# Performance work log

Hardware: AMD Instinct MI355X
Metric: run time of the kernel (lower is better)

The kernel has to match this reference:

```python
import jax, jax.numpy as jnp
import numpy as np

NS, NV = 48, 10                    # scalar / vector multiplicities (cfg.ns, cfg.nv)
WN = NS * NS + NS * NV             # per-edge TP weight numel: paths 0e*0e->0e and 0e*1o->1o
OUT = NS + 3 * NV                  # out irreps 48x0e + 10x1o -> 78 dims
INV = float(1.0 / np.sqrt(NS))     # e3nn-style path normalization (fan_in = mul_in)
N_LIG, N_REC, N_ATOM = 2000, 2000, 15000
E_LL, E_RR, E_AA = 15000, 10000, 15000
E_LR, E_LA, E_AR = 5000, 8000, 8000


def setup_inputs() -> dict:
    key = jax.random.key(0)
    ks = jax.random.split(key, 40)
    f = lambda i, shape, s=1.0: jax.random.normal(ks[i], shape, dtype=jnp.float32) * s
    ii = lambda i, n, e: jax.random.randint(ks[i], (e,), 0, n, dtype=jnp.int32)
    w_s = (1.0 / (3 * NS)) ** 0.5
    return {
        'lig_x': f(0, (N_LIG, NS)), 'rec_x': f(1, (N_REC, NS)), 'atom_x': f(2, (N_ATOM, NS)),
        'll_attr': f(3, (E_LL, NS)), 'rr_attr': f(4, (E_RR, NS)), 'aa_attr': f(5, (E_AA, NS)),
        'lr_attr': f(6, (E_LR, NS)), 'la_attr': f(7, (E_LA, NS)), 'ar_attr': f(8, (E_AR, NS)),
        'll_sh': f(9, (E_LL, 9)), 'rr_sh': f(10, (E_RR, 9)), 'aa_sh': f(11, (E_AA, 9)),
        'lr_sh': f(12, (E_LR, 9)), 'la_sh': f(13, (E_LA, 9)), 'ar_sh': f(14, (E_AR, 9)),
        'mlp_w1': f(15, (9, 3 * NS, 3 * NS), w_s), 'mlp_b1': jnp.zeros((9, 3 * NS), jnp.float32),
        'mlp_w2': f(16, (9, 3 * NS, 3 * NS), w_s), 'mlp_b2': jnp.zeros((9, 3 * NS), jnp.float32),
        'mlp_w3': f(17, (9, 3 * NS, WN), w_s), 'mlp_b3': jnp.zeros((9, WN), jnp.float32),
        'll_src': ii(18, N_LIG, E_LL), 'll_dst': ii(19, N_LIG, E_LL),
        'rr_src': ii(20, N_REC, E_RR), 'rr_dst': ii(21, N_REC, E_RR),
        'aa_src': ii(22, N_ATOM, E_AA), 'aa_dst': ii(23, N_ATOM, E_AA),
        'lr_lig': ii(24, N_LIG, E_LR), 'lr_rec': ii(25, N_REC, E_LR),
        'la_lig': ii(26, N_LIG, E_LA), 'la_atom': ii(27, N_ATOM, E_LA),
        'ar_atom': ii(28, N_ATOM, E_AR), 'ar_rec': ii(29, N_REC, E_AR),
    }


def _tp_conv(src_x, dst_x, e_attr, e_sh, src_idx, dst_idx, n_dst, w1, b1, w2, b2, w3, b3):
    """FullyConnectedTensorProductConv: per-edge MLP -> TP weights, CG tensor
    product of gathered source features with edge SH, mean scatter to dst."""
    fs = src_x[src_idx]                                          # (E, ns) gather
    z = jnp.concatenate([e_attr, fs, dst_x[dst_idx]], axis=-1)
    h = jax.nn.relu(z @ w1 + b1)
    h = jax.nn.relu(h @ w2 + b2)
    w = h @ w3 + b3                                              # (E, WN) edge-conditioned TP weights
    w0 = w[:, : NS * NS].reshape(-1, NS, NS)                     # 0e x 0e -> 0e path
    wv = w[:, NS * NS :].reshape(-1, NS, NV)                     # 0e x 1o -> 1o path
    out0 = jnp.einsum('ei,eio->eo', fs, w0) * e_sh[:, :1] * INV  # (E, ns)
    outv = jnp.einsum('ei,eiv,em->evm', fs, wv, e_sh[:, 1:4]) * INV  # (E, nv, 3)
    msg = jnp.concatenate([out0, outv.reshape(-1, NV * 3)], axis=-1)
    agg = jax.ops.segment_sum(msg, dst_idx, num_segments=n_dst)
    deg = jax.ops.segment_sum(jnp.ones((msg.shape[0], 1), msg.dtype), dst_idx, num_segments=n_dst)
    return agg / jnp.maximum(deg, 1.0)                           # mean reduction


def reference(lig_x, rec_x, atom_x, ll_attr, rr_attr, aa_attr, lr_attr, la_attr, ar_attr,
              ll_sh, rr_sh, aa_sh, lr_sh, la_sh, ar_sh,
              mlp_w1, mlp_b1, mlp_w2, mlp_b2, mlp_w3, mlp_b3,
              ll_src, ll_dst, rr_src, rr_dst, aa_src, aa_dst,
              lr_lig, lr_rec, la_lig, la_atom, ar_atom, ar_rec):
    P = lambda c: (mlp_w1[c], mlp_b1[c], mlp_w2[c], mlp_b2[c], mlp_w3[c], mlp_b3[c])
    # one interaction layer = 9 structurally distinct convs (lig/rec/atom intra + 6 cross dirs)
    lig_u = (_tp_conv(lig_x, lig_x, ll_attr, ll_sh, ll_src, ll_dst, N_LIG, *P(0))
           + _tp_conv(rec_x, lig_x, lr_attr, lr_sh, lr_rec, lr_lig, N_LIG, *P(1))
           + _tp_conv(atom_x, lig_x, la_attr, la_sh, la_atom, la_lig, N_LIG, *P(2)))
    rec_u = (_tp_conv(lig_x, rec_x, lr_attr, lr_sh, lr_lig, lr_rec, N_REC, *P(3))
           + _tp_conv(rec_x, rec_x, rr_attr, rr_sh, rr_src, rr_dst, N_REC, *P(4))
           + _tp_conv(atom_x, rec_x, ar_attr, ar_sh, ar_atom, ar_rec, N_REC, *P(5)))
    atom_u = (_tp_conv(lig_x, atom_x, la_attr, la_sh, la_lig, la_atom, N_ATOM, *P(6))
            + _tp_conv(rec_x, atom_x, ar_attr, ar_sh, ar_rec, ar_atom, N_ATOM, *P(7))
            + _tp_conv(atom_x, atom_x, aa_attr, aa_sh, aa_src, aa_dst, N_ATOM, *P(8)))
    pad = lambda x: jnp.pad(x, ((0, 0), (0, OUT - NS)))          # residual: pad scalars to out irreps
    return jnp.concatenate([pad(lig_x) + lig_u, pad(rec_x) + rec_u, pad(atom_x) + atom_u], axis=0)
```

## Files before the change

kernel.cpp:

```cpp
#include <hip/hip_runtime.h>


namespace {

constexpr int NCONV = 9;
constexpr int ETOT  = 82000;
constexpr float INV = 0.14433756729740643f;

constexpr int EC[NCONV]     = {15000,5000,8000,5000,10000,8000,8000,8000,15000};
constexpr int NBLKC[NCONV]  = {118,40,63,40,79,63,63,63,118};
constexpr int EOFF[NCONV]   = {0,15000,20000,28000,33000,43000,51000,59000,67000};
constexpr int DEGOFF[NCONV] = {0,2000,4000,6000,8000,10000,12000,27000,42000};
constexpr int NODEC[NCONV]  = {2000,2000,2000,2000,2000,2000,15000,15000,15000};
constexpr int NBLK_TOT = 647;

typedef _Float16 f16;
typedef __attribute__((ext_vector_type(8))) _Float16 f16x8;
typedef __attribute__((ext_vector_type(4))) _Float16 f16x4;
typedef __attribute__((ext_vector_type(4))) float f32x4;

#define MFMA(a, b, c) __builtin_amdgcn_mfma_f32_16x16x32_f16((a), (b), (c), 0, 0, 0)

struct ConvPtrs {
  const float* src_x[NCONV];
  const float* dst_x[NCONV];
  const float* attr[NCONV];
  const float* sh[NCONV];
  const int*   sidx[NCONV];
  const int*   didx[NCONV];
};

}

__device__ __forceinline__ int xcd_remap(int bid) {
  const int xcd = bid & 7, slot = bid >> 3;
  return (xcd <= 6) ? (xcd * 81 + slot) : (567 + slot);
}

__device__ __forceinline__ int conv_decode(int bid, int& rem) {
  int c = 0; rem = bid;
  while (c < NCONV - 1 && rem >= NBLKC[c]) { rem -= NBLKC[c]; ++c; }
  return c;
}

__device__ __forceinline__ void gld_lds16(const void* g, void* l) {
  __builtin_amdgcn_global_load_lds(
      (const __attribute__((address_space(1))) void*)g,
      (__attribute__((address_space(3))) void*)l, 16, 0, 0);
}

__device__ __forceinline__ f32x4 cvt4(f16x4 h) {
  return (f32x4){(float)h[0], (float)h[1], (float)h[2], (float)h[3]};
}

__global__ __launch_bounds__(256) void prep_all(
    ConvPtrs P,
    const float* __restrict__ w1, const float* __restrict__ b1,
    const float* __restrict__ w2, const float* __restrict__ b2,
    const float* __restrict__ w3, const float* __restrict__ b3,
    f16* __restrict__ w1f, f16* __restrict__ w2f, f16* __restrict__ w3f,
    float* __restrict__ deg) {
  __shared__ float W[145][60];
  const int blk = blockIdx.x;
  if (blk < 203) {
    const int unit = blk * 4 + (threadIdx.x >> 6);
    if (unit >= 810) return;
    const int l = threadIdx.x & 63;
    const int sel = unit >= 405, bb = sel ? unit - 405 : unit;
    const int c = bb / 45, r2 = bb % 45, cb = r2 / 5, s = r2 % 5;
    const float* w  = sel ? w2 : w1;
    const float* bi = sel ? b2 : b1;
    f16* dst = (sel ? w2f : w1f) + ((size_t)(c * 9 + cb) * 5 + s) * 512;
    const int n = cb * 16 + (l & 15);
    f16x8 pack;
#pragma unroll
    for (int j = 0; j < 8; ++j) {
      const int k = s * 32 + ((l >> 4) << 3) + j;
      float v = 0.f;
      if (k < 144)       v = w[((size_t)c * 144 + k) * 144 + n];
      else if (k == 144) v = bi[c * 144 + n];
      pack[j] = (f16)v;
    }
    ((f16x8*)dst)[l] = pack;
  } else if (blk < 635) {
    const int b = blk - 203;
    const int c = b / 48, i = b % 48;
    const float* wc = w3 + (size_t)c * 144 * 2784;
    const float* bc = b3 + (size_t)c * 2784;
    for (int u = threadIdx.x; u < 145 * 58; u += 256) {
      const int row = u / 58, t = u - row * 58;
      const int col = (t < 48) ? (i * 48 + t) : (2304 + i * 10 + (t - 48));
      const float* src = (row == 144) ? bc : (wc + (size_t)row * 2784);
      W[row][t] = src[col];
    }
    __syncthreads();
    f16* dst = w3f + (size_t)(c * 48 + i) * 20 * 512;
#pragma unroll 1
    for (int it = 0; it < 40; ++it) {
      const int f = it * 256 + threadIdx.x;
      const int s = f >> 11, g2 = f & 2047, cb = g2 >> 9, l = (g2 >> 3) & 63, j = f & 7;
      const int k = s * 32 + ((l >> 4) << 3) + j;
      const int col = cb * 16 + (l & 15);
      const float v = (k <= 144 && col < 58) ? W[k][col] : 0.f;
      dst[f] = (f16)v;
    }
  } else {
    const int gid = (blk - 635) * 256 + threadIdx.x;
    if (gid >= ETOT) return;
    int c = 0;
    while (c < NCONV - 1 && gid >= EOFF[c + 1]) ++c;
    const int e = gid - EOFF[c];
    atomicAdd(&deg[DEGOFF[c] + P.didx[c][e]], 1.0f);
  }
}

__global__ __launch_bounds__(256) void scan_kernel(
    const float* __restrict__ deg, int* __restrict__ offs, int* __restrict__ cursor) {
  __shared__ int part[256];
  const int c = blockIdx.x, N = NODEC[c], base = DEGOFF[c];
  const int tid = threadIdx.x;
  const int chunk = (N + 255) / 256;
  const int start = tid * chunk;
  const int end = (start + chunk < N) ? (start + chunk) : N;
  int s = 0;
  for (int i = start; i < end; ++i) s += (int)deg[base + i];
  part[tid] = s;
  __syncthreads();
  if (tid == 0) {
    int acc = 0;
    for (int k = 0; k < 256; ++k) { int t = part[k]; part[k] = acc; acc += t; }
  }
  __syncthreads();
  int acc = part[tid];
  for (int i = start; i < end; ++i) {
    offs[base + i] = acc; cursor[base + i] = acc;
    acc += (int)deg[base + i];
  }
}

__global__ __launch_bounds__(256) void slot_kernel(
    ConvPtrs P, int* __restrict__ cursor, int* __restrict__ inv_slot) {
  const int gid = blockIdx.x * 256 + threadIdx.x;
  if (gid >= ETOT) return;
  int c = 0;
  while (c < NCONV - 1 && gid >= EOFF[c + 1]) ++c;
  const int e = gid - EOFF[c];
  const int d = P.didx[c][e];
  inv_slot[gid] = atomicAdd(&cursor[DEGOFF[c] + d], 1);
}

template<int NCB, int CB0>
__device__ __forceinline__ void layer_mm(
    const f16x8* __restrict__ Av, const f16x8* __restrict__ wv,
    int c, int lane, int wr, f32x4 acc[4][5]) {
#pragma unroll
  for (int rb = 0; rb < 4; ++rb)
#pragma unroll
    for (int cb = 0; cb < NCB; ++cb) acc[rb][cb] = (f32x4)0.0f;
#pragma unroll
  for (int s = 0; s < 5; ++s) {
    f16x8 B[NCB];
#pragma unroll
    for (int cb = 0; cb < NCB; ++cb)
      B[cb] = wv[((size_t)(c * 9 + CB0 + cb) * 5 + s) * 64 + lane];
    f16x8 A[4];
#pragma unroll
    for (int rb = 0; rb < 4; ++rb) A[rb] = Av[((wr * 4 + rb) * 5 + s) * 64 + lane];
#pragma unroll
    for (int rb = 0; rb < 4; ++rb)
#pragma unroll
      for (int cb = 0; cb < NCB; ++cb)
        acc[rb][cb] = MFMA(A[rb], B[cb], acc[rb][cb]);
  }
}

template<int NCB, int CB0>
__device__ __forceinline__ void layer_wb(const f32x4 acc[4][5], f16* __restrict__ At,
                                         int lane, int wr) {
#pragma unroll
  for (int cb = 0; cb < NCB; ++cb) {
    const int k = (CB0 + cb) * 16 + (lane & 15);
    const int s = k >> 5, g = (k >> 3) & 3, j = k & 7;
#pragma unroll
    for (int rb = 0; rb < 4; ++rb)
#pragma unroll
      for (int r = 0; r < 4; ++r) {
        const int row = ((lane >> 4) << 2) + r;
        At[((((wr * 4 + rb) * 5 + s) * 4 + g) * 16 + row) * 8 + j] =
            (f16)fmaxf(acc[rb][cb][r], 0.f);
      }
  }
}

__global__ __launch_bounds__(256, 3) void fused_conv(
    ConvPtrs P, const f16* __restrict__ w1f, const f16* __restrict__ w2f,
    const f16* __restrict__ w3f, const float* __restrict__ deg,
    const int* __restrict__ inv_slot, f16* __restrict__ medge) {
  __shared__ __align__(16) char smem[54272];
  f16* Atile = (f16*)smem;
  f16 (*fst)[128] = (f16 (*)[128])(smem + 40960);
  int* sidb = (int*)(smem + 53248);
  int* dstb = (int*)(smem + 53760);

  int rem; const int c = conv_decode(xcd_remap(blockIdx.x), rem);
  const int E = EC[c], e0 = rem * 128;
  const int tid = threadIdx.x, lane = tid & 63, w = tid >> 6;
  const int wr = w >> 1, wc = w & 1;

  if (tid < 128) {
    int ec = e0 + tid; if (ec >= E) ec = E - 1;
    sidb[tid] = P.sidx[c][ec];
    dstb[tid] = P.didx[c][ec];
  }
  __syncthreads();

  {
    const float* attr = P.attr[c];
    const float* sx = P.src_x[c];
    const float* dx = P.dst_x[c];
#pragma unroll 1
    for (int it = 0; it < 10; ++it) {
      const int u = it * 256 + tid, j8 = u >> 7, e = u & 127;
      int ec = e0 + e; if (ec >= E) ec = E - 1;
      float v[8];
      if (j8 < 6) {
        const float* p = attr + (size_t)ec * 48 + j8 * 8;
#pragma unroll
        for (int t = 0; t < 8; ++t) v[t] = p[t];
      } else if (j8 < 12) {
        const float* p = sx + (size_t)sidb[e] * 48 + (j8 - 6) * 8;
#pragma unroll
        for (int t = 0; t < 8; ++t) v[t] = p[t];
#pragma unroll
        for (int t = 0; t < 8; ++t) fst[(j8 - 6) * 8 + t][e] = (f16)v[t];
      } else if (j8 < 18) {
        const float* p = dx + (size_t)dstb[e] * 48 + (j8 - 12) * 8;
#pragma unroll
        for (int t = 0; t < 8; ++t) v[t] = p[t];
      } else if (j8 == 18) {
        v[0] = 1.f;
#pragma unroll
        for (int t = 1; t < 8; ++t) v[t] = 0.f;
      } else {
#pragma unroll
        for (int t = 0; t < 8; ++t) v[t] = 0.f;
      }
      f16x8 h;
#pragma unroll
      for (int t = 0; t < 8; ++t) h[t] = (f16)v[t];
      const int s = j8 >> 2, g = j8 & 3, rbg = e >> 4, row = e & 15;
      ((f16x8*)Atile)[((rbg * 5 + s) * 4 + g) * 16 + row] = h;
    }
  }
  __syncthreads();

  const f16x8* Av = (const f16x8*)Atile;

  f32x4 acc[4][5];
  if (wc == 0) layer_mm<5, 0>(Av, (const f16x8*)w1f, c, lane, wr, acc);
  else         layer_mm<4, 5>(Av, (const f16x8*)w1f, c, lane, wr, acc);
  __syncthreads();
  if (wc == 0) layer_wb<5, 0>(acc, Atile, lane, wr);
  else         layer_wb<4, 5>(acc, Atile, lane, wr);
  __syncthreads();
  if (wc == 0) layer_mm<5, 0>(Av, (const f16x8*)w2f, c, lane, wr, acc);
  else         layer_mm<4, 5>(Av, (const f16x8*)w2f, c, lane, wr, acc);
  __syncthreads();
  if (wc == 0) layer_wb<5, 0>(acc, Atile, lane, wr);
  else         layer_wb<4, 5>(acc, Atile, lane, wr);
  __syncthreads();

  f16x8 Af[4][5];
#pragma unroll
  for (int rb = 0; rb < 4; ++rb)
#pragma unroll
    for (int s = 0; s < 5; ++s)
      Af[rb][s] = Av[((wr * 4 + rb) * 5 + s) * 64 + lane];
  __syncthreads();

  const f16* __restrict__ w3c = w3f + (size_t)(c * 48) * 10240;
  f16* buf0 = Atile;
  f16* buf1 = Atile + 10240;

  f32x4 msg[4][2];
#pragma unroll
  for (int rb = 0; rb < 4; ++rb)
#pragma unroll
    for (int cb = 0; cb < 2; ++cb) msg[rb][cb] = (f32x4)0.0f;

#pragma unroll
  for (int q = 0; q < 5; ++q) {
    const int chunk = q * 4 + w;
    gld_lds16(w3c + chunk * 512 + lane * 8, buf0 + chunk * 512);
  }
  __syncthreads();

#pragma unroll 1
  for (int i = 0; i < 48; ++i) {
    f16* bcur = (i & 1) ? buf1 : buf0;
    f16* bnxt = (i & 1) ? buf0 : buf1;
    if (i + 1 < 48) {
      const f16* gsrc = w3c + (size_t)(i + 1) * 10240;
#pragma unroll
      for (int q = 0; q < 5; ++q) {
        const int chunk = q * 4 + w;
        gld_lds16(gsrc + chunk * 512 + lane * 8, bnxt + chunk * 512);
      }
    }
    f16x4 fsh[4];
#pragma unroll
    for (int rb = 0; rb < 4; ++rb)
      fsh[rb] = *(const f16x4*)&fst[i][wr * 64 + rb * 16 + ((lane >> 4) << 2)];

    const f16x8* bv = (const f16x8*)bcur;
#pragma unroll
    for (int cb = 0; cb < 2; ++cb) {
      f16x8 Bf[5];
#pragma unroll
      for (int s = 0; s < 5; ++s) Bf[s] = bv[(s * 4 + wc * 2 + cb) * 64 + lane];
      f32x4 T[4];
#pragma unroll
      for (int rb = 0; rb < 4; ++rb) T[rb] = (f32x4)0.0f;
#pragma unroll
      for (int s = 0; s < 5; ++s)
#pragma unroll
        for (int rb = 0; rb < 4; ++rb) T[rb] = MFMA(Af[rb][s], Bf[s], T[rb]);
#pragma unroll
      for (int rb = 0; rb < 4; ++rb) msg[rb][cb] += cvt4(fsh[rb]) * T[rb];
    }
    __syncthreads();
  }

  const float* __restrict__ shp = P.sh[c];
  const float* __restrict__ degc = deg + DEGOFF[c];
#pragma unroll
  for (int rb = 0; rb < 4; ++rb)
#pragma unroll
    for (int r = 0; r < 4; ++r) {
      const int el = wr * 64 + rb * 16 + ((lane >> 4) << 2) + r;
      const int ec = e0 + el;
      if (ec >= E) continue;
      const int dst = dstb[el];
      const float sc = INV / fmaxf(degc[dst], 1.f);
      const float* shq = shp + (size_t)ec * 9;
      const float s0 = shq[0], s1 = shq[1], s2 = shq[2], s3 = shq[3];
      const int pos = inv_slot[EOFF[c] + ec];
      f16* mp = medge + (size_t)(EOFF[c] + pos) * 80;
#pragma unroll
      for (int cb = 0; cb < 2; ++cb) {
        const int col = (wc * 2 + cb) * 16 + (lane & 15);
        const float v = msg[rb][cb][r] * sc;
        if (col < 48) {
          mp[col] = (f16)(v * s0);
        } else if (col < 58) {
          const int vv = col - 48;
          mp[48 + vv * 3 + 0] = (f16)(v * s1);
          mp[48 + vv * 3 + 1] = (f16)(v * s2);
          mp[48 + vv * 3 + 2] = (f16)(v * s3);
        }
      }
    }
}

__global__ __launch_bounds__(256) void finalize_kernel(
    const float* __restrict__ lig, const float* __restrict__ rec,
    const float* __restrict__ atom, const int* __restrict__ offs,
    const int* __restrict__ cursor, const f16* __restrict__ medge,
    float* __restrict__ out) {
  const int tid = threadIdx.x;
  if (tid >= 240) return;
  const int r3 = tid / 80, j = tid - r3 * 80;
  const int row = blockIdx.x * 3 + r3;
  if (row >= 19000 || j >= 78) return;
  int node, cb; const float* x;
  if (row < 2000)      { node = row;        cb = 0; x = lig; }
  else if (row < 4000) { node = row - 2000; cb = 3; x = rec; }
  else                 { node = row - 4000; cb = 6; x = atom; }
  float r = (j < 48) ? x[(size_t)node * 48 + j] : 0.f;
#pragma unroll
  for (int t = 0; t < 3; ++t) {
    const int c = cb + t;
    const int base = DEGOFF[c] + node;
    const int o = offs[base], e = cursor[base];
    for (int k = o; k < e; ++k)
      r += (float)medge[(size_t)(EOFF[c] + k) * 80 + j];
  }
  out[(size_t)row * 78 + j] = r;
}

extern "C" void kernel_launch(void* const* d_in, const int* in_sizes, int n_in,
                              void* d_out, int out_size, void* d_ws, size_t ws_size,
                              hipStream_t stream) {
  (void)in_sizes; (void)n_in; (void)out_size; (void)ws_size;
  const float* lig_x  = (const float*)d_in[0];
  const float* rec_x  = (const float*)d_in[1];
  const float* atom_x = (const float*)d_in[2];
  const float* attr_ll = (const float*)d_in[3];
  const float* attr_rr = (const float*)d_in[4];
  const float* attr_aa = (const float*)d_in[5];
  const float* attr_lr = (const float*)d_in[6];
  const float* attr_la = (const float*)d_in[7];
  const float* attr_ar = (const float*)d_in[8];
  const float* sh_ll = (const float*)d_in[9];
  const float* sh_rr = (const float*)d_in[10];
  const float* sh_aa = (const float*)d_in[11];
  const float* sh_lr = (const float*)d_in[12];
  const float* sh_la = (const float*)d_in[13];
  const float* sh_ar = (const float*)d_in[14];
  const float* w1 = (const float*)d_in[15];
  const float* b1 = (const float*)d_in[16];
  const float* w2 = (const float*)d_in[17];
  const float* b2 = (const float*)d_in[18];
  const float* w3 = (const float*)d_in[19];
  const float* b3 = (const float*)d_in[20];
  const int* ll_src = (const int*)d_in[21];
  const int* ll_dst = (const int*)d_in[22];
  const int* rr_src = (const int*)d_in[23];
  const int* rr_dst = (const int*)d_in[24];
  const int* aa_src = (const int*)d_in[25];
  const int* aa_dst = (const int*)d_in[26];
  const int* lr_lig = (const int*)d_in[27];
  const int* lr_rec = (const int*)d_in[28];
  const int* la_lig = (const int*)d_in[29];
  const int* la_atom = (const int*)d_in[30];
  const int* ar_atom = (const int*)d_in[31];
  const int* ar_rec  = (const int*)d_in[32];

  f16* w1f = (f16*)d_ws;
  f16* w2f = w1f + 207360;
  f16* w3f = w2f + 207360;
  float* deg     = (float*)(w3f + 4423680);
  int*   offs    = (int*)(deg + 57000);
  int*   cursor  = offs + 57000;
  int*   inv_slot= cursor + 57000;
  f16*   medge   = (f16*)(inv_slot + 82000);

  ConvPtrs P;
  const float* SX[NCONV] = {lig_x, rec_x, atom_x, lig_x, rec_x, atom_x, lig_x, rec_x, atom_x};
  const float* DX[NCONV] = {lig_x, lig_x, lig_x, rec_x, rec_x, rec_x, atom_x, atom_x, atom_x};
  const float* AT[NCONV] = {attr_ll, attr_lr, attr_la, attr_lr, attr_rr, attr_ar, attr_la, attr_ar, attr_aa};
  const float* SH[NCONV] = {sh_ll, sh_lr, sh_la, sh_lr, sh_rr, sh_ar, sh_la, sh_ar, sh_aa};
  const int*   SI[NCONV] = {ll_src, lr_rec, la_atom, lr_lig, rr_src, ar_atom, la_lig, ar_rec, aa_src};
  const int*   DI[NCONV] = {ll_dst, lr_lig, la_lig, lr_rec, rr_dst, ar_rec, la_atom, ar_atom, aa_dst};
  for (int cc = 0; cc < NCONV; ++cc) {
    P.src_x[cc] = SX[cc]; P.dst_x[cc] = DX[cc]; P.attr[cc] = AT[cc];
    P.sh[cc] = SH[cc]; P.sidx[cc] = SI[cc]; P.didx[cc] = DI[cc];
  }

  hipMemsetAsync(deg, 0, 57000 * sizeof(float), stream);
  prep_all<<<956, 256, 0, stream>>>(P, w1, b1, w2, b2, w3, b3, w1f, w2f, w3f, deg);
  scan_kernel<<<NCONV, 256, 0, stream>>>(deg, offs, cursor);
  slot_kernel<<<(ETOT + 255) / 256, 256, 0, stream>>>(P, cursor, inv_slot);
  fused_conv<<<NBLK_TOT, 256, 0, stream>>>(P, w1f, w2f, w3f, deg, inv_slot, medge);
  finalize_kernel<<<(19000 + 2) / 3, 256, 0, stream>>>(lig_x, rec_x, atom_x, offs,
                                                       cursor, medge, (float*)d_out);
}
```

Measured before the change: 204.7 us.

## Split fused conv into MLP and bilinear kernels with split-barrier weight pipeline

Splits the fused conv kernel in two. The first kernel runs the two MLP layers and writes the hidden activations and gathered source features to global scratch. The second kernel reloads them and streams the third-layer weights through a double-buffered LDS ring, using explicit s_barrier, partial vmcnt waits and raised wave priority around the MFMA step. This aims to overlap the next weight tile load with compute and to free the bilinear loop from the MLP's register and LDS pressure. The cost is an extra global round-trip of roughly 26 MB of intermediates plus one more kernel launch.

After: 192.9 us. -5.8%, faster.

```diff
diff --git a/kernel.cpp b/kernel.cpp
--- a/kernel.cpp
+++ b/kernel.cpp
@@ -192,17 +192,17 @@
   }
 }
 
-__global__ __launch_bounds__(256, 3) void fused_conv(
+__global__ __launch_bounds__(256, 3) void mlp_kernel(
     ConvPtrs P, const f16* __restrict__ w1f, const f16* __restrict__ w2f,
-    const f16* __restrict__ w3f, const float* __restrict__ deg,
-    const int* __restrict__ inv_slot, f16* __restrict__ medge) {
+    f16* __restrict__ h2g, f16* __restrict__ fstg) {
   __shared__ __align__(16) char smem[54272];
   f16* Atile = (f16*)smem;
   f16 (*fst)[128] = (f16 (*)[128])(smem + 40960);
   int* sidb = (int*)(smem + 53248);
   int* dstb = (int*)(smem + 53760);
 
-  int rem; const int c = conv_decode(xcd_remap(blockIdx.x), rem);
+  const int f = xcd_remap(blockIdx.x);
+  int rem; const int c = conv_decode(f, rem);
   const int E = EC[c], e0 = rem * 128;
   const int tid = threadIdx.x, lane = tid & 63, w = tid >> 6;
   const int wr = w >> 1, wc = w & 1;
@@ -255,7 +255,6 @@
   __syncthreads();
 
   const f16x8* Av = (const f16x8*)Atile;
-
   f32x4 acc[4][5];
   if (wc == 0) layer_mm<5, 0>(Av, (const f16x8*)w1f, c, lane, wr, acc);
   else         layer_mm<4, 5>(Av, (const f16x8*)w1f, c, lane, wr, acc);
@@ -270,69 +269,107 @@
   else         layer_wb<4, 5>(acc, Atile, lane, wr);
   __syncthreads();
 
+  const f16x8* As = (const f16x8*)Atile;
+  f16x8* hd = (f16x8*)(h2g + (size_t)f * 20480);
+#pragma unroll
+  for (int t = 0; t < 10; ++t) hd[t * 256 + tid] = As[t * 256 + tid];
+  const f16x8* fs8 = (const f16x8*)fst;
+  f16x8* fd = (f16x8*)(fstg + (size_t)f * 6144);
+#pragma unroll
+  for (int t = 0; t < 3; ++t) fd[t * 256 + tid] = fs8[t * 256 + tid];
+}
+
+__device__ __forceinline__ void bilin_step(
+    const f16* __restrict__ slot, const f16 (*fstl)[128], int i,
+    const f16x8 Af[4][5], f32x4 msg[4][2], int lane, int wr, int wc) {
+  f16x4 fsh[4];
+#pragma unroll
+  for (int rb = 0; rb < 4; ++rb)
+    fsh[rb] = *(const f16x4*)&fstl[i][wr * 64 + rb * 16 + ((lane >> 4) << 2)];
+  const f16x8* bv = (const f16x8*)slot;
+  __builtin_amdgcn_s_setprio(1);
+#pragma unroll
+  for (int cb = 0; cb < 2; ++cb) {
+    f16x8 Bf[5];
+#pragma unroll
+    for (int s = 0; s < 5; ++s) Bf[s] = bv[(s * 4 + wc * 2 + cb) * 64 + lane];
+    f32x4 T[4];
+#pragma unroll
+    for (int rb = 0; rb < 4; ++rb) T[rb] = (f32x4)0.0f;
+#pragma unroll
+    for (int s = 0; s < 5; ++s)
+#pragma unroll
+      for (int rb = 0; rb < 4; ++rb) T[rb] = MFMA(Af[rb][s], Bf[s], T[rb]);
+#pragma unroll
+    for (int rb = 0; rb < 4; ++rb) msg[rb][cb] += cvt4(fsh[rb]) * T[rb];
+  }
+  __builtin_amdgcn_s_setprio(0);
+}
+
+__global__ __launch_bounds__(256, 3) void bilin_kernel(
+    ConvPtrs P, const f16* __restrict__ w3f, const f16* __restrict__ h2g,
+    const f16* __restrict__ fstg, const float* __restrict__ deg,
+    const int* __restrict__ inv_slot, f16* __restrict__ medge) {
+  __shared__ __align__(16) char smem[53248];
+  f16* ring = (f16*)smem;
+  f16 (*fstl)[128] = (f16 (*)[128])(smem + 40960);
+
+  const int f = xcd_remap(blockIdx.x);
+  int rem; const int c = conv_decode(f, rem);
+  const int E = EC[c], e0 = rem * 128;
+  const int tid = threadIdx.x, lane = tid & 63, w = tid >> 6;
+  const int wr = w >> 1, wc = w & 1;
+
+  const f16x8* hv = (const f16x8*)(h2g + (size_t)f * 20480);
   f16x8 Af[4][5];
 #pragma unroll
   for (int rb = 0; rb < 4; ++rb)
 #pragma unroll
     for (int s = 0; s < 5; ++s)
-      Af[rb][s] = Av[((wr * 4 + rb) * 5 + s) * 64 + lane];
-  __syncthreads();
-
+      Af[rb][s] = hv[((wr * 4 + rb) * 5 + s) * 64 + lane];
+
+  const f16* fsrc = fstg + (size_t)f * 6144;
+#pragma unroll
+  for (int t = 0; t < 3; ++t) {
+    const int chunk = w * 3 + t;
+    gld_lds16(fsrc + chunk * 512 + lane * 8, ((f16*)fstl) + chunk * 512);
+  }
   const f16* __restrict__ w3c = w3f + (size_t)(c * 48) * 10240;
-  f16* buf0 = Atile;
-  f16* buf1 = Atile + 10240;
-
-  f32x4 msg[4][2];
-#pragma unroll
-  for (int rb = 0; rb < 4; ++rb)
-#pragma unroll
-    for (int cb = 0; cb < 2; ++cb) msg[rb][cb] = (f32x4)0.0f;
-
 #pragma unroll
   for (int q = 0; q < 5; ++q) {
     const int chunk = q * 4 + w;
-    gld_lds16(w3c + chunk * 512 + lane * 8, buf0 + chunk * 512);
-  }
-  __syncthreads();
+    gld_lds16(w3c + chunk * 512 + lane * 8, ring + chunk * 512);
+  }
+
+  f32x4 msg[4][2];
+#pragma unroll
+  for (int rb = 0; rb < 4; ++rb)
+#pragma unroll
+    for (int cb = 0; cb < 2; ++cb) msg[rb][cb] = (f32x4)0.0f;
 
 #pragma unroll 1
-  for (int i = 0; i < 48; ++i) {
-    f16* bcur = (i & 1) ? buf1 : buf0;
-    f16* bnxt = (i & 1) ? buf0 : buf1;
-    if (i + 1 < 48) {
-      const f16* gsrc = w3c + (size_t)(i + 1) * 10240;
-#pragma unroll
-      for (int q = 0; q < 5; ++q) {
-        const int chunk = q * 4 + w;
-        gld_lds16(gsrc + chunk * 512 + lane * 8, bnxt + chunk * 512);
-      }
-    }
-    f16x4 fsh[4];
-#pragma unroll
-    for (int rb = 0; rb < 4; ++rb)
-      fsh[rb] = *(const f16x4*)&fst[i][wr * 64 + rb * 16 + ((lane >> 4) << 2)];
-
-    const f16x8* bv = (const f16x8*)bcur;
-#pragma unroll
-    for (int cb = 0; cb < 2; ++cb) {
-      f16x8 Bf[5];
-#pragma unroll
-      for (int s = 0; s < 5; ++s) Bf[s] = bv[(s * 4 + wc * 2 + cb) * 64 + lane];
-      f32x4 T[4];
-#pragma unroll
-      for (int rb = 0; rb < 4; ++rb) T[rb] = (f32x4)0.0f;
-#pragma unroll
-      for (int s = 0; s < 5; ++s)
-#pragma unroll
-        for (int rb = 0; rb < 4; ++rb) T[rb] = MFMA(Af[rb][s], Bf[s], T[rb]);
-#pragma unroll
-      for (int rb = 0; rb < 4; ++rb) msg[rb][cb] += cvt4(fsh[rb]) * T[rb];
-    }
-    __syncthreads();
-  }
+  for (int i = 0; i < 47; ++i) {
+    __builtin_amdgcn_s_barrier();
+    const f16* gsrc = w3c + (size_t)(i + 1) * 10240;
+    f16* bdst = ring + ((i + 1) & 1) * 10240;
+#pragma unroll
+    for (int q = 0; q < 5; ++q) {
+      const int chunk = q * 4 + w;
+      gld_lds16(gsrc + chunk * 512 + lane * 8, bdst + chunk * 512);
+    }
+    asm volatile("s_waitcnt vmcnt(5)" ::: "memory");
+    __builtin_amdgcn_s_barrier();
+    __builtin_amdgcn_sched_barrier(0);
+    bilin_step(ring + (i & 1) * 10240, fstl, i, Af, msg, lane, wr, wc);
+  }
+  __builtin_amdgcn_s_barrier();
+  asm volatile("s_waitcnt vmcnt(0)" ::: "memory");
+  __builtin_amdgcn_s_barrier();
+  bilin_step(ring + (47 & 1) * 10240, fstl, 47, Af, msg, lane, wr, wc);
 
   const float* __restrict__ shp = P.sh[c];
   const float* __restrict__ degc = deg + DEGOFF[c];
+  const int* __restrict__ didx = P.didx[c];
 #pragma unroll
   for (int rb = 0; rb < 4; ++rb)
 #pragma unroll
@@ -340,8 +377,7 @@
       const int el = wr * 64 + rb * 16 + ((lane >> 4) << 2) + r;
       const int ec = e0 + el;
       if (ec >= E) continue;
-      const int dst = dstb[el];
-      const float sc = INV / fmaxf(degc[dst], 1.f);
+      const float sc = INV / fmaxf(degc[didx[ec]], 1.f);
       const float* shq = shp + (size_t)ec * 9;
       const float s0 = shq[0], s1 = shq[1], s2 = shq[2], s3 = shq[3];
       const int pos = inv_slot[EOFF[c] + ec];
@@ -434,6 +470,8 @@
   int*   cursor  = offs + 57000;
   int*   inv_slot= cursor + 57000;
   f16*   medge   = (f16*)(inv_slot + 82000);
+  f16*   h2g     = medge + 6560000;
+  f16*   fstg    = h2g + 13250560;
 
   ConvPtrs P;
   const float* SX[NCONV] = {lig_x, rec_x, atom_x, lig_x, rec_x, atom_x, lig_x, rec_x, atom_x};
@@ -451,7 +489,8 @@
   prep_all<<<956, 256, 0, stream>>>(P, w1, b1, w2, b2, w3, b3, w1f, w2f, w3f, deg);
   scan_kernel<<<NCONV, 256, 0, stream>>>(deg, offs, cursor);
   slot_kernel<<<(ETOT + 255) / 256, 256, 0, stream>>>(P, cursor, inv_slot);
-  fused_conv<<<NBLK_TOT, 256, 0, stream>>>(P, w1f, w2f, w3f, deg, inv_slot, medge);
+  mlp_kernel<<<NBLK_TOT, 256, 0, stream>>>(P, w1f, w2f, h2g, fstg);
+  bilin_kernel<<<NBLK_TOT, 256, 0, stream>>>(P, w3f, h2g, fstg, deg, inv_slot, medge);
   finalize_kernel<<<(19000 + 2) / 3, 256, 0, stream>>>(lig_x, rec_x, atom_x, offs,
                                                        cursor, medge, (float*)d_out);
 }
```
